# Kernel optimization log

Hardware: AMD Instinct MI355X
Metric: run time of the kernel (lower is better)

## Reference

```python
import jax, jax.numpy as jnp
import numpy as np
import math

B, L, D, H, DFF, NL = 32, 512, 768, 12, 3072, 2
E = D // H
VOCAB = 30522
TOPK = int(1 * math.log(L))   # factor=1 -> 6
MA = 25                        # series_decomp moving-average kernel (Autoformer default)
CMID = D // 2                  # 384 conv channels
PLEN = (L - 2) // 2            # 255 pooled length
LATENT, NCELLS = 32, 2034


def _ln(x, g, b, eps=1e-5):
    mu = x.mean(-1, keepdims=True)
    v = ((x - mu) ** 2).mean(-1, keepdims=True)
    return (x - mu) * jax.lax.rsqrt(v + eps) * g + b


def _decomp(x):
    # series_decomp: x - moving_avg(x, k=25) with replicate padding, via cumsum
    pad = (MA - 1) // 2
    xp = jnp.concatenate([jnp.repeat(x[:, :1], pad, 1), x, jnp.repeat(x[:, -1:], pad, 1)], 1)
    cs = jnp.cumsum(xp, axis=1)
    cs = jnp.concatenate([jnp.zeros_like(cs[:, :1]), cs], 1)
    mm = (cs[:, MA:] - cs[:, :-MA]) / MA  # [B,L,D]
    return x - mm


def _autocorr(q, k, v):
    # q,k,v: [B,L,H,E] -> FFT autocorrelation + top-k delay aggregation (inference path)
    qt = jnp.transpose(q, (0, 2, 3, 1))
    kt = jnp.transpose(k, (0, 2, 3, 1))
    vt = jnp.transpose(v, (0, 2, 3, 1))  # [B,H,E,L]
    corr = jnp.fft.irfft(jnp.fft.rfft(qt, axis=-1) * jnp.conj(jnp.fft.rfft(kt, axis=-1)), n=L, axis=-1)
    mean_value = corr.mean(axis=(1, 2))                      # [B,L]
    weights, delay = jax.lax.top_k(mean_value, TOPK)         # [B,K]
    w = jax.nn.softmax(weights, axis=-1)                     # [B,K]
    tv = jnp.concatenate([vt, vt], -1)                       # [B,H,E,2L]
    idx = jnp.arange(L)[None, None, :] + delay[:, :, None]   # [B,K,L]
    pat = jnp.take_along_axis(tv[:, None], idx[:, :, None, None, :], axis=-1)  # [B,K,H,E,L]
    V = jnp.einsum('bkhel,bk->bhel', pat, w)
    return jnp.transpose(V, (0, 3, 1, 2))                    # [B,L,H,E]


def _forward(input_ids, word_emb, pos_emb, tok_emb, emb_ln_g, emb_ln_b,
             Wq, bq, Wk, bk, Wv, bv, Wo, bo, Wc1, bc1, Wc2, bc2,
             norm_g, norm_b, conv_w, conv_b, bn_g, bn_b, bn_m, bn_v,
             lin1_w, lin1_b, ln2_g, ln2_b, lin2_w, lin2_b):
    # BertEmbeddings (token_type all zeros)
    x = word_emb[input_ids] + pos_emb[None, :L] + tok_emb[0][None, None]
    x = _ln(x, emb_ln_g, emb_ln_b, 1e-12)
    # Autoformer encoder layers
    for l in range(NL):
        q = (x @ Wq[l].T + bq[l]).reshape(B, L, H, E)
        k = (x @ Wk[l].T + bk[l]).reshape(B, L, H, E)
        v = (x @ Wv[l].T + bv[l]).reshape(B, L, H, E)
        a = _autocorr(q, k, v).reshape(B, L, D) @ Wo[l].T + bo[l]
        x = _decomp(x + a)
        y = jax.nn.gelu(x @ Wc1[l].T + bc1[l], approximate=False) @ Wc2[l].T + bc2[l]
        x = _decomp(x + y)
    # my_Layernorm
    x_hat = _ln(x, norm_g, norm_b)
    att_out = x_hat - x_hat.mean(axis=1, keepdims=True)      # [B,L,D]
    # Prediction head
    z = jnp.transpose(att_out, (0, 2, 1))                    # [B,D,L]
    c = jax.lax.conv_general_dilated(z, conv_w, (1,), 'VALID',
                                     dimension_numbers=('NCH', 'OIH', 'NCH')) + conv_b[None, :, None]
    c = (c - bn_m[None, :, None]) * jax.lax.rsqrt(bn_v + 1e-5)[None, :, None] * bn_g[None, :, None] + bn_b[None, :, None]
    c = jax.nn.elu(c)                                        # [B,384,510]
    p = c.reshape(B, CMID, PLEN, 2).max(-1)                  # maxpool k=2
    f = p.reshape(B, CMID * PLEN)
    h = jax.nn.elu(_ln(f @ lin1_w.T + lin1_b, ln2_g, ln2_b))
    return jax.nn.sigmoid(h @ lin2_w.T + lin2_b)             # [B,2034]


def setup_inputs() -> dict:
    key = jax.random.key(0)
    ks = iter(jax.random.split(key, 64))
    n = lambda *s: 0.02 * jax.random.normal(next(ks), s, dtype=jnp.float32)
    return dict(
        input_ids=jax.random.randint(next(ks), (B, L), 0, VOCAB),
        word_emb=n(VOCAB, D), pos_emb=n(L, D), tok_emb=n(2, D),
        emb_ln_g=jnp.ones((D,), jnp.float32), emb_ln_b=jnp.zeros((D,), jnp.float32),
        Wq=n(NL, D, D), bq=n(NL, D), Wk=n(NL, D, D), bk=n(NL, D),
        Wv=n(NL, D, D), bv=n(NL, D), Wo=n(NL, D, D), bo=n(NL, D),
        Wc1=n(NL, DFF, D), bc1=n(NL, DFF), Wc2=n(NL, D, DFF), bc2=n(NL, D),
        norm_g=jnp.ones((D,), jnp.float32), norm_b=jnp.zeros((D,), jnp.float32),
        conv_w=n(CMID, D, 3), conv_b=n(CMID),
        bn_g=jnp.ones((CMID,), jnp.float32), bn_b=jnp.zeros((CMID,), jnp.float32),
        bn_m=n(CMID), bn_v=jax.random.uniform(next(ks), (CMID,), jnp.float32) + 0.5,
        lin1_w=n(LATENT, CMID * PLEN), lin1_b=n(LATENT),
        ln2_g=jnp.ones((LATENT,), jnp.float32), ln2_b=jnp.zeros((LATENT,), jnp.float32),
        lin2_w=n(NCELLS, LATENT), lin2_b=n(NCELLS),
    )


def reference(input_ids, word_emb, pos_emb, tok_emb, emb_ln_g, emb_ln_b,
              Wq, bq, Wk, bk, Wv, bv, Wo, bo, Wc1, bc1, Wc2, bc2,
              norm_g, norm_b, conv_w, conv_b, bn_g, bn_b, bn_m, bn_v,
              lin1_w, lin1_b, ln2_g, ln2_b, lin2_w, lin2_b):
    return _forward(input_ids, word_emb, pos_emb, tok_emb, emb_ln_g, emb_ln_b,
                    Wq, bq, Wk, bk, Wv, bv, Wo, bo, Wc1, bc1, Wc2, bc2,
                    norm_g, norm_b, conv_w, conv_b, bn_g, bn_b, bn_m, bn_v,
                    lin1_w, lin1_b, ln2_g, ln2_b, lin2_w, lin2_b)
```

## Files before the change

kernel.cpp:

```cpp
#include <hip/hip_runtime.h>
#include <hip/hip_bf16.h>

#define B_ 32
#define L_ 512
#define D_ 768
#define DFF_ 3072
#define NL_ 2
#define TOPK_ 6
#define CMID_ 384
#define CLEN_ 510
#define PLEN_ 255
#define LATENT_ 32
#define NCELLS_ 2034
#define NROWS_ (B_*L_)
#define ND_ ((size_t)B_*L_*D_)

typedef unsigned short ushort_t;
typedef __attribute__((ext_vector_type(8))) short short8;
typedef __attribute__((ext_vector_type(4))) float f32x4;

typedef const __attribute__((address_space(1))) unsigned int* gp1;
typedef __attribute__((address_space(3))) unsigned int* lp3;

static __device__ __forceinline__ void gload16(const ushort_t* g, ushort_t* l) {
  __builtin_amdgcn_global_load_lds((gp1)g, (lp3)l, 16, 0, 0);
}

static __device__ __forceinline__ float geluf(float x) {
  return 0.5f * x * (1.f + erff(x * 0.70710678118654752440f));
}
static __device__ __forceinline__ float eluf(float x) {
  return x > 0.f ? x : expm1f(x);
}
static __device__ __forceinline__ ushort_t bf16rn(float f) {
  unsigned u = __builtin_bit_cast(unsigned, f);
  u = u + 0x7FFFu + ((u >> 16) & 1u);
  return (ushort_t)(u >> 16);
}
static __device__ __forceinline__ float bf16tof(ushort_t s) {
  unsigned u = ((unsigned)s) << 16;
  return __builtin_bit_cast(float, u);
}
static __device__ __forceinline__ f32x4 mfma16(short8 a, short8 b, f32x4 c) {
  return __builtin_amdgcn_mfma_f32_16x16x32_bf16(a, b, c, 0, 0, 0);
}

__global__ void wsplit(const float* __restrict__ w, ushort_t* __restrict__ hi,
                       ushort_t* __restrict__ lo, size_t n) {
  size_t stride = (size_t)gridDim.x * blockDim.x;
  for (size_t i = (size_t)blockIdx.x * blockDim.x + threadIdx.x; i < n; i += stride) {
    float v = w[i];
    ushort_t h = bf16rn(v);
    hi[i] = h;
    if (lo) lo[i] = bf16rn(v - bf16tof(h));
  }
}

__global__ __launch_bounds__(256) void tsplit(const float* __restrict__ in, ushort_t* __restrict__ hiT,
                                              ushort_t* __restrict__ loT) {
  __shared__ float tile[32][33];
  size_t off = (size_t)blockIdx.z * D_ * D_;
  int bx = blockIdx.x * 32, by = blockIdx.y * 32;
  int tx = threadIdx.x & 31, ty = threadIdx.x >> 5;
#pragma unroll
  for (int i = 0; i < 32; i += 8)
    tile[ty + i][tx] = in[off + (size_t)(by + ty + i) * D_ + bx + tx];
  __syncthreads();
#pragma unroll
  for (int i = 0; i < 32; i += 8) {
    float v = tile[tx][ty + i];
    ushort_t h = bf16rn(v);
    size_t o = off + (size_t)(bx + ty + i) * D_ + by + tx;
    hiT[o] = h;
    loT[o] = bf16rn(v - bf16tof(h));
  }
}

__global__ void bvo_k(const float* __restrict__ wo, const float* __restrict__ bv,
                      const float* __restrict__ bo, float* __restrict__ bvo) {
  int gid = blockIdx.x * 256 + threadIdx.x;
  if (gid >= NL_ * D_) return;
  int l = gid / D_, a = gid % D_;
  const float* w = wo + (size_t)l * D_ * D_ + (size_t)a * D_;
  const float* b = bv + l * D_;
  float s = bo[gid];
  for (int j = 0; j < D_; j++) s = fmaf(w[j], b[j], s);
  bvo[gid] = s;
}

__global__ void conv_w_repack(const float* __restrict__ w, ushort_t* __restrict__ wt) {
  int gid = blockIdx.x * blockDim.x + threadIdx.x;
  if (gid >= CMID_ * 3 * D_) return;
  int o = gid / (3 * D_);
  int k = gid % (3 * D_);
  int j = k / D_, i = k % D_;
  wt[gid] = bf16rn(w[((size_t)o * D_ + i) * 3 + j]);
}

__global__ __launch_bounds__(256) void embed_ln(const int* __restrict__ ids, const float* __restrict__ we,
                                                const float* __restrict__ pe, const float* __restrict__ te,
                                                const float* __restrict__ g, const float* __restrict__ bta,
                                                ushort_t* __restrict__ xh, ushort_t* __restrict__ xl) {
  int row = blockIdx.x;
  int tid = threadIdx.x;
  int t = row & (L_ - 1);
  int id = ids[row];
  float v[3];
#pragma unroll
  for (int dd = 0; dd < 3; dd++) {
    int c = tid + dd * 256;
    v[dd] = we[(size_t)id * D_ + c] + pe[(size_t)t * D_ + c] + te[c];
  }
  float s = v[0] + v[1] + v[2];
  float sq = v[0]*v[0] + v[1]*v[1] + v[2]*v[2];
  __shared__ float rs[256], rq[256];
  rs[tid] = s; rq[tid] = sq;
  __syncthreads();
  for (int st = 128; st > 0; st >>= 1) {
    if (tid < st) { rs[tid] += rs[tid + st]; rq[tid] += rq[tid + st]; }
    __syncthreads();
  }
  __shared__ float smu, ssc;
  if (tid == 0) {
    float mu = rs[0] * (1.f / D_);
    float var = fmaxf(rq[0] * (1.f / D_) - mu * mu, 0.f);
    smu = mu; ssc = rsqrtf(var + 1e-12f);
  }
  __syncthreads();
  float mu = smu, sc = ssc;
#pragma unroll
  for (int dd = 0; dd < 3; dd++) {
    int c = tid + dd * 256;
    size_t o = (size_t)row * D_ + c;
    float ov = (v[dd] - mu) * sc * g[c] + bta[c];
    ushort_t h = bf16rn(ov);
    xh[o] = h;
    xl[o] = bf16rn(ov - bf16tof(h));
  }
}

__global__ __launch_bounds__(256) void ln_pl(const ushort_t* __restrict__ xh, const ushort_t* __restrict__ xl,
                                             float* __restrict__ out,
                                             const float* __restrict__ g, const float* __restrict__ bta,
                                             float eps) {
  int row = blockIdx.x;
  int tid = threadIdx.x;
  size_t base = (size_t)row * D_;
  float v[3];
#pragma unroll
  for (int dd = 0; dd < 3; dd++) {
    size_t o = base + tid + dd * 256;
    v[dd] = bf16tof(xh[o]) + bf16tof(xl[o]);
  }
  float s = v[0] + v[1] + v[2];
  float sq = v[0]*v[0] + v[1]*v[1] + v[2]*v[2];
  __shared__ float rs[256], rq[256];
  rs[tid] = s; rq[tid] = sq;
  __syncthreads();
  for (int st = 128; st > 0; st >>= 1) {
    if (tid < st) { rs[tid] += rs[tid + st]; rq[tid] += rq[tid + st]; }
    __syncthreads();
  }
  __shared__ float smu, ssc;
  if (tid == 0) {
    float mu = rs[0] * (1.f / D_);
    float var = fmaxf(rq[0] * (1.f / D_) - mu * mu, 0.f);
    smu = mu; ssc = rsqrtf(var + eps);
  }
  __syncthreads();
  float mu = smu, sc = ssc;
  float* o = out + base;
#pragma unroll
  for (int dd = 0; dd < 3; dd++) {
    int c = tid + dd * 256;
    o[c] = (v[dd] - mu) * sc * g[c] + bta[c];
  }
}

template<int ACT, int EPI>
__global__ __launch_bounds__(512, 1) void gemm8p(
    const ushort_t* __restrict__ A, const ushort_t* __restrict__ W,
    const float* __restrict__ bias,
    const ushort_t* __restrict__ ResH, const ushort_t* __restrict__ ResL,
    void* __restrict__ C0, int O, int K, int lda, int nbx, int nby) {
  __shared__ __align__(16) ushort_t Asm[2][16384];
  __shared__ __align__(16) ushort_t Bsm[2][16384];

  int nwg = gridDim.x;
  int wg = blockIdx.x;
  {
    int qq = nwg >> 3, rr = nwg & 7;
    int xcd = wg & 7, idx = wg >> 3;
    wg = (xcd < rr ? xcd * (qq + 1) : rr * (qq + 1) + (xcd - rr) * qq) + idx;
  }
  int gsz = nbx * 8;
  int grp = wg / gsz;
  int ing = wg - grp * gsz;
  int by0 = grp * 8;
  int gmx = min(8, nby - by0);
  int by = by0 + (ing % gmx);
  int bx = ing / gmx;

  int m0 = by * 256, o0 = bx * 256;
  int tid = threadIdx.x;
  int wave = tid >> 6, lane = tid & 63;
  int wm = wave >> 2, wn = wave & 3;
  int lcol = lane & 15, lk = lane >> 4;
  int swzl = (lcol & 3) ^ ((lcol >> 2) & 3);
  int sloA = ((lk ^ swzl) << 3);
  int srcsw = (((tid & 3) ^ ((tid >> 2) & 3) ^ ((tid >> 4) & 3)) << 3);
  int nt = K >> 6;
  int niter = nt >> 1;

  f32x4 acc[8][4] = {};

  auto STAGE = [&](int T, int mat, int kh) {
    if (T >= nt) return;
    ushort_t* lb = (mat == 0 ? &Asm[T & 1][kh * 8192 + (wave << 9)]
                             : &Bsm[T & 1][kh * 8192 + (wave << 9)]);
    const ushort_t* gb = (mat == 0 ? A : W);
    int ld = (mat == 0 ? lda : K);
    int br = (mat == 0 ? m0 : o0) + (tid >> 2);
    int cc = T * 64 + kh * 32 + srcsw;
    gload16(gb + (size_t)br * ld + cc, lb);
    gload16(gb + (size_t)(br + 128) * ld + cc, lb + 4096);
  };

#define PHASE_(bufi, mh, kh, sT, sM, sK)                                         \
  {                                                                              \
    short8 af[4], bfr[4];                                                        \
    _Pragma("unroll")                                                            \
    for (int fi = 0; fi < 4; fi++)                                               \
      af[fi] = *(const short8*)&Asm[bufi][(kh) * 8192 +                          \
               (wm * 128 + (mh) * 64 + fi * 16 + lcol) * 32 + sloA];             \
    _Pragma("unroll")                                                            \
    for (int fj = 0; fj < 4; fj++)                                               \
      bfr[fj] = *(const short8*)&Bsm[bufi][(kh) * 8192 +                         \
               (wn * 64 + fj * 16 + lcol) * 32 + sloA];                          \
    STAGE(sT, sM, sK);                                                           \
    __builtin_amdgcn_s_barrier();                                                \
    asm volatile("s_waitcnt lgkmcnt(0)" ::: "memory");                           \
    __builtin_amdgcn_sched_barrier(0);                                           \
    __builtin_amdgcn_s_setprio(1);                                               \
    _Pragma("unroll")                                                            \
    for (int fi = 0; fi < 4; fi++)                                               \
      _Pragma("unroll")                                                          \
      for (int fj = 0; fj < 4; fj++)                                             \
        acc[(mh) * 4 + fi][fj] = mfma16(af[fi], bfr[fj], acc[(mh) * 4 + fi][fj]);\
    __builtin_amdgcn_s_setprio(0);                                               \
    __builtin_amdgcn_s_barrier();                                                \
  }

  STAGE(0, 0, 0); STAGE(0, 1, 0); STAGE(0, 0, 1); STAGE(0, 1, 1);
  STAGE(1, 0, 0); STAGE(1, 1, 0);

  for (int i = 0; i < niter; i++) {
    int E = 2 * i;
    asm volatile("s_waitcnt vmcnt(4)" ::: "memory");
    __builtin_amdgcn_s_barrier();
    PHASE_(0, 0, 0, E + 1, 0, 1);
    PHASE_(0, 1, 0, E + 1, 1, 1);
    PHASE_(0, 0, 1, E + 2, 0, 0);
    PHASE_(0, 1, 1, E + 2, 1, 0);
    if (i + 1 == niter) asm volatile("s_waitcnt vmcnt(0)" ::: "memory");
    else                asm volatile("s_waitcnt vmcnt(4)" ::: "memory");
    __builtin_amdgcn_s_barrier();
    PHASE_(1, 0, 0, E + 2, 0, 1);
    PHASE_(1, 1, 0, E + 2, 1, 1);
    PHASE_(1, 0, 1, E + 3, 0, 0);
    PHASE_(1, 1, 1, E + 3, 1, 0);
  }
#undef PHASE_

#pragma unroll
  for (int fi = 0; fi < 8; fi++) {
    int rowb = m0 + wm * 128 + fi * 16 + lk * 4;
#pragma unroll
    for (int fj = 0; fj < 4; fj++) {
      int col = o0 + wn * 64 + fj * 16 + lcol;
      float bv = bias ? bias[col] : 0.f;
#pragma unroll
      for (int r = 0; r < 4; r++) {
        float v = acc[fi][fj][r] + bv;
        if (ACT == 1) v = geluf(v);
        size_t off = (size_t)(rowb + r) * O + col;
        if (EPI == 0) {
          if (ResH) v += bf16tof(ResH[off]) + bf16tof(ResL[off]);
          ((float*)C0)[off] = v;
        }
        if (EPI == 1) ((ushort_t*)C0)[off] = bf16rn(v);
      }
    }
  }
}

template<int ACT, bool SPLIT, int EPI>
__global__ __launch_bounds__(256) void gemm_bf16(
    const ushort_t* __restrict__ Ah, const ushort_t* __restrict__ Al,
    const ushort_t* __restrict__ Wh, const ushort_t* __restrict__ Wl,
    const float* __restrict__ bias,
    const ushort_t* __restrict__ ResH, const ushort_t* __restrict__ ResL,
    void* __restrict__ C0, void* __restrict__ C1,
    const float* __restrict__ bn_m, const float* __restrict__ bn_v,
    const float* __restrict__ bn_g, const float* __restrict__ bn_b,
    int O, int K, int lda,
    long long sA, long long sW, long long sC,
    int nbx, int nby) {
  constexpr int NP = SPLIT ? 2 : 1;
  __shared__ __align__(16) ushort_t AsH[NP][128 * 64];
  __shared__ __align__(16) ushort_t WsH[NP][128 * 64];
  __shared__ float dsum[EPI == 3 ? 512 : 1];

  int nwg = gridDim.x;
  int wg = blockIdx.x;
  {
    int qq = nwg >> 3, rr = nwg & 7;
    int xcd = wg & 7, idx = wg >> 3;
    wg = (xcd < rr ? xcd * (qq + 1) : rr * (qq + 1) + (xcd - rr) * qq) + idx;
  }
  int per_b = nbx * nby;
  int bz = wg / per_b;
  int rem = wg - bz * per_b;
  int gsz = nbx * 8;
  int grp = rem / gsz;
  int ing = rem - grp * gsz;
  int by0 = grp * 8;
  int gmx = min(8, nby - by0);
  int by = by0 + (ing % gmx);
  int bx = ing / gmx;

  const ushort_t* Ahb = Ah + (size_t)bz * sA;
  const ushort_t* Alb = SPLIT ? (Al + (size_t)bz * sA) : nullptr;
  const ushort_t* Whb = Wh + (size_t)bz * sW;
  const ushort_t* Wlb = SPLIT ? (Wl + (size_t)bz * sW) : nullptr;

  int m0 = by * 128, o0 = bx * 128;
  int tid = threadIdx.x;
  int wave = tid >> 6, lane = tid & 63;
  int wm = (wave >> 1) * 64, wn = (wave & 1) * 64;
  int lcol = lane & 15, lk = lane >> 4;

  if (EPI == 3) {
    for (int s = tid; s < 512; s += 256) dsum[s] = 0.f;
  }

  f32x4 acc[4][4] = {};

  int r8 = lane >> 3;
  int kc = (((lane & 7) ^ r8) << 3);

  const ushort_t *gA[4], *gW[4], *gAl[4], *gWl[4];
#pragma unroll
  for (int i = 0; i < 4; i++) {
    int ch = wave * 4 + i;
    int row = ch * 8 + r8;
    size_t oa = (size_t)(m0 + row) * lda + kc;
    size_t ow = (size_t)(o0 + row) * K + kc;
    gA[i] = Ahb + oa; gW[i] = Whb + ow;
    if (SPLIT) { gAl[i] = Alb + oa; gWl[i] = Wlb + ow; }
  }

  for (int k0 = 0; k0 < K; k0 += 64) {
#pragma unroll
    for (int i = 0; i < 4; i++) {
      int ch = wave * 4 + i;
      gload16(gA[i], &AsH[0][ch * 512]); gA[i] += 64;
      gload16(gW[i], &WsH[0][ch * 512]); gW[i] += 64;
      if (SPLIT) {
        gload16(gAl[i], &AsH[1][ch * 512]); gAl[i] += 64;
        gload16(gWl[i], &WsH[1][ch * 512]); gWl[i] += 64;
      }
    }
    __syncthreads();
#pragma unroll
    for (int kk = 0; kk < 2; kk++) {
      int c = kk * 4 + lk;
      short8 ah[4], bh[4], al[4], bl[4];
#pragma unroll
      for (int i = 0; i < 4; i++) {
        int r = wm + i * 16 + lcol;
        int so = r * 64 + ((c ^ (r & 7)) << 3);
        ah[i] = *(const short8*)&AsH[0][so];
        if (SPLIT) al[i] = *(const short8*)&AsH[1][so];
      }
#pragma unroll
      for (int j = 0; j < 4; j++) {
        int r = wn + j * 16 + lcol;
        int so = r * 64 + ((c ^ (r & 7)) << 3);
        bh[j] = *(const short8*)&WsH[0][so];
        if (SPLIT) bl[j] = *(const short8*)&WsH[1][so];
      }
#pragma unroll
      for (int i = 0; i < 4; i++)
#pragma unroll
        for (int j = 0; j < 4; j++) {
          if (SPLIT) {
            acc[i][j] = mfma16(ah[i], bl[j], acc[i][j]);
            acc[i][j] = mfma16(al[i], bh[j], acc[i][j]);
          }
          acc[i][j] = mfma16(ah[i], bh[j], acc[i][j]);
        }
    }
    __syncthreads();
  }

  if (EPI == 3) {
    float pre[7][4] = {};
#pragma unroll
    for (int i = 0; i < 4; i++)
#pragma unroll
      for (int j = 0; j < 4; j++)
#pragma unroll
        for (int r = 0; r < 4; r++)
          pre[i - j + 3][r] += acc[i][j][r];
    int base = (m0 + wm + lk * 4) - (o0 + wn + lcol);
#pragma unroll
    for (int g = 0; g < 7; g++)
#pragma unroll
      for (int r = 0; r < 4; r++)
        atomicAdd(&dsum[(base + 16 * (g - 3) + r) & (L_ - 1)], pre[g][r]);
    __syncthreads();
    float* mvp = (float*)C0;
    int blk = by * nbx + bx;
    for (int s = tid; s < 512; s += 256)
      mvp[((size_t)bz * 16 + blk) * 512 + s] = dsum[s] * (1.f / D_);
  } else if (EPI == 4) {
#pragma unroll
    for (int j = 0; j < 4; j++) {
      int col = o0 + wn + j * 16 + lcol;
      float cbias = bias[col];
      float sc = rsqrtf(bn_v[col] + 1e-5f) * bn_g[col];
      float shf = bn_b[col] - bn_m[col] * sc;
#pragma unroll
      for (int i = 0; i < 4; i++) {
        int rowb = m0 + wm + i * 16 + lk * 4;
        int t = rowb & (L_ - 1);
        int b = rowb >> 9;
#pragma unroll
        for (int p = 0; p < 2; p++) {
          int tt = t + p * 2;
          if (tt >= CLEN_) continue;
          float v0 = eluf((acc[i][j][p * 2]     + cbias) * sc + shf);
          float v1 = eluf((acc[i][j][p * 2 + 1] + cbias) * sc + shf);
          ((float*)C0)[((size_t)b * CMID_ + col) * PLEN_ + (tt >> 1)] = fmaxf(v0, v1);
        }
      }
    }
  } else {
#pragma unroll
    for (int i = 0; i < 4; i++)
#pragma unroll
      for (int j = 0; j < 4; j++) {
        int col = o0 + wn + j * 16 + lcol;
        float bv = bias ? bias[col] : 0.f;
        int rowb = m0 + wm + i * 16 + lk * 4;
#pragma unroll
        for (int r = 0; r < 4; r++) {
          float v = acc[i][j][r] + bv;
          if (ACT == 1) v = geluf(v);
          size_t off = (size_t)bz * sC + (size_t)(rowb + r) * O + col;
          if (EPI == 0) {
            if (ResH) v += bf16tof(ResH[off]) + bf16tof(ResL[off]);
            ((float*)C0)[off] = v;
          }
          if (EPI == 1) ((ushort_t*)C0)[off] = bf16rn(v);
          if (EPI == 2) {
            ushort_t h = bf16rn(v);
            ((ushort_t*)C0)[off] = h;
            ((ushort_t*)C1)[off] = bf16rn(v - bf16tof(h));
          }
        }
      }
  }
}

__global__ __launch_bounds__(256) void topk_softmax(const float* __restrict__ mvp,
                                                    float* __restrict__ wout, int* __restrict__ dout) {
  int b = blockIdx.x, tid = threadIdx.x;
  __shared__ float vals[L_];
  __shared__ float rv[256];
  __shared__ int ri[256];
  __shared__ float wsel[TOPK_];
  __shared__ int dsel[TOPK_];
  float s0 = 0.f, s1 = 0.f;
  for (int p = 0; p < 16; p++) {
    const float* pp = mvp + ((size_t)b * 16 + p) * L_;
    s0 += pp[tid]; s1 += pp[tid + 256];
  }
  vals[tid] = s0; vals[tid + 256] = s1;
  for (int kk = 0; kk < TOPK_; kk++) {
    __syncthreads();
    float v0 = vals[tid], v1 = vals[tid + 256];
    float bvv = v0; int bi = tid;
    if (v1 > v0) { bvv = v1; bi = tid + 256; }
    rv[tid] = bvv; ri[tid] = bi;
    __syncthreads();
    for (int st = 128; st > 0; st >>= 1) {
      if (tid < st) {
        float ov = rv[tid + st]; int oi = ri[tid + st];
        if (ov > rv[tid] || (ov == rv[tid] && oi < ri[tid])) { rv[tid] = ov; ri[tid] = oi; }
      }
      __syncthreads();
    }
    if (tid == 0) { wsel[kk] = rv[0]; dsel[kk] = ri[0]; vals[ri[0]] = -INFINITY; }
  }
  __syncthreads();
  if (tid == 0) {
    float mx = wsel[0];
    for (int i = 1; i < TOPK_; i++) mx = fmaxf(mx, wsel[i]);
    float e[TOPK_]; float sum = 0.f;
    for (int i = 0; i < TOPK_; i++) { e[i] = expf(wsel[i] - mx); sum += e[i]; }
    for (int i = 0; i < TOPK_; i++) { wout[b * TOPK_ + i] = e[i] / sum; dout[b * TOPK_ + i] = dsel[i]; }
  }
}

__global__ __launch_bounds__(256) void agg_res(const ushort_t* __restrict__ P, const float* __restrict__ w,
                                               const int* __restrict__ dly,
                                               const ushort_t* __restrict__ xh, const ushort_t* __restrict__ xl,
                                               float* __restrict__ y) {
  int blr = blockIdx.x;
  int b = blr >> 9, t = blr & 511;
  int tid = threadIdx.x;
  __shared__ float ww[TOPK_];
  __shared__ int rr[TOPK_];
  if (tid < TOPK_) { ww[tid] = w[b * TOPK_ + tid]; rr[tid] = (t + dly[b * TOPK_ + tid]) & (L_ - 1); }
  __syncthreads();
  const ushort_t* pb = P + (size_t)b * L_ * D_;
#pragma unroll
  for (int dd = 0; dd < 3; dd++) {
    int d = tid + dd * 256;
    size_t o = (size_t)blr * D_ + d;
    float s = bf16tof(xh[o]) + bf16tof(xl[o]);
#pragma unroll
    for (int kk = 0; kk < TOPK_; kk++)
      s = fmaf(ww[kk], bf16tof(pb[(size_t)rr[kk] * D_ + d]), s);
    y[o] = s;
  }
}

__global__ void decomp_pl(const float* __restrict__ s,
                          ushort_t* __restrict__ xh, ushort_t* __restrict__ xl) {
  int gid = blockIdx.x * blockDim.x + threadIdx.x;
  if (gid >= B_ * 8 * D_) return;
  int d = gid % D_;
  int chunk = (gid / D_) & 7;
  int b = gid / (D_ * 8);
  size_t base = (size_t)b * L_ * D_ + d;
  int t0 = chunk * 64;
  float wsum = 0.f;
  for (int u = t0 - 12; u <= t0 + 12; u++) {
    int uc = u < 0 ? 0 : (u > L_ - 1 ? L_ - 1 : u);
    wsum += s[base + (size_t)uc * D_];
  }
  for (int t = t0; t < t0 + 64; t++) {
    size_t o = base + (size_t)t * D_;
    float v = s[o] - wsum * (1.f / 25.f);
    ushort_t h = bf16rn(v);
    xh[o] = h;
    xl[o] = bf16rn(v - bf16tof(h));
    int ua = t + 13 > L_ - 1 ? L_ - 1 : t + 13;
    int ur = t - 12 < 0 ? 0 : t - 12;
    wsum += s[base + (size_t)ua * D_] - s[base + (size_t)ur * D_];
  }
}

__global__ void colmean_bf16(const float* __restrict__ x, ushort_t* __restrict__ sh) {
  int gid = blockIdx.x * blockDim.x + threadIdx.x;
  if (gid >= B_ * D_) return;
  int d = gid % D_, b = gid / D_;
  const float* col = x + (size_t)b * L_ * D_ + d;
  ushort_t* oc = sh + (size_t)b * L_ * D_ + d;
  float s = 0.f;
  for (int t = 0; t < L_; t++) s += col[(size_t)t * D_];
  float mu = s * (1.f / L_);
  for (int t = 0; t < L_; t++) oc[(size_t)t * D_] = bf16rn(col[(size_t)t * D_] - mu);
}

__global__ __launch_bounds__(256) void lin1_k(const float* __restrict__ f, const float* __restrict__ w,
                                              const float* __restrict__ bias, float* __restrict__ out) {
  int o = blockIdx.x, b = blockIdx.y;
  int tid = threadIdx.x;
  const float4* fr = (const float4*)(f + (size_t)b * (CMID_ * PLEN_));
  const float4* wr = (const float4*)(w + (size_t)o * (CMID_ * PLEN_));
  const int n4 = CMID_ * PLEN_ / 4;
  float s = 0.f;
  for (int i = tid; i < n4; i += 256) {
    float4 a = fr[i], ww = wr[i];
    s += a.x * ww.x + a.y * ww.y + a.z * ww.z + a.w * ww.w;
  }
  __shared__ float red[256];
  red[tid] = s;
  __syncthreads();
  for (int st = 128; st > 0; st >>= 1) {
    if (tid < st) red[tid] += red[tid + st];
    __syncthreads();
  }
  if (tid == 0) out[b * LATENT_ + o] = red[0] + bias[o];
}

__global__ void ln_elu(const float* __restrict__ hp, const float* __restrict__ g,
                       const float* __restrict__ bb, float* __restrict__ h) {
  int b = blockIdx.x;
  int tid = threadIdx.x;
  __shared__ float v[LATENT_];
  __shared__ float mu_s, sc_s;
  if (tid < LATENT_) v[tid] = hp[b * LATENT_ + tid];
  __syncthreads();
  if (tid == 0) {
    float s = 0.f, sq = 0.f;
    for (int i = 0; i < LATENT_; i++) { s += v[i]; sq += v[i] * v[i]; }
    float mu = s * (1.f / LATENT_);
    float var = fmaxf(sq * (1.f / LATENT_) - mu * mu, 0.f);
    mu_s = mu; sc_s = rsqrtf(var + 1e-5f);
  }
  __syncthreads();
  if (tid < LATENT_) h[b * LATENT_ + tid] = eluf((v[tid] - mu_s) * sc_s * g[tid] + bb[tid]);
}

__global__ void lin2_sig(const float* __restrict__ h, const float* __restrict__ w,
                         const float* __restrict__ bias, float* __restrict__ out) {
  int gid = blockIdx.x * blockDim.x + threadIdx.x;
  if (gid >= B_ * NCELLS_) return;
  int b = gid / NCELLS_, c = gid % NCELLS_;
  const float* hr = h + b * LATENT_;
  const float* wr = w + (size_t)c * LATENT_;
  float s = bias[c];
  for (int j = 0; j < LATENT_; j++) s = fmaf(hr[j], wr[j], s);
  out[gid] = 1.f / (1.f + expf(-s));
}

extern "C" void kernel_launch(void* const* d_in, const int* in_sizes, int n_in,
                              void* d_out, int out_size, void* d_ws, size_t ws_size,
                              hipStream_t stream) {
  const int*   ids  = (const int*)  d_in[0];
  const float* we   = (const float*)d_in[1];
  const float* pe   = (const float*)d_in[2];
  const float* te   = (const float*)d_in[3];
  const float* elng = (const float*)d_in[4];
  const float* elnb = (const float*)d_in[5];
  const float* Wq   = (const float*)d_in[6];
  const float* bq   = (const float*)d_in[7];   (void)bq;
  const float* Wk   = (const float*)d_in[8];
  const float* bk   = (const float*)d_in[9];   (void)bk;
  const float* Wv   = (const float*)d_in[10];
  const float* bv   = (const float*)d_in[11];
  const float* Wo   = (const float*)d_in[12];
  const float* bo   = (const float*)d_in[13];
  const float* Wc1  = (const float*)d_in[14];
  const float* bc1  = (const float*)d_in[15];
  const float* Wc2  = (const float*)d_in[16];
  const float* bc2  = (const float*)d_in[17];
  const float* ng   = (const float*)d_in[18];
  const float* nb   = (const float*)d_in[19];
  const float* cw   = (const float*)d_in[20];
  const float* cb   = (const float*)d_in[21];
  const float* bng  = (const float*)d_in[22];
  const float* bnb  = (const float*)d_in[23];
  const float* bnm  = (const float*)d_in[24];
  const float* bnv  = (const float*)d_in[25];
  const float* l1w  = (const float*)d_in[26];
  const float* l1b  = (const float*)d_in[27];
  const float* l2g  = (const float*)d_in[28];
  const float* l2b  = (const float*)d_in[29];
  const float* l2w  = (const float*)d_in[30];
  const float* l2bi = (const float*)d_in[31];
  float* out = (float*)d_out;

  char* wp = (char*)d_ws;
  auto alloc = [&](size_t bytes) { char* p = wp; wp += (bytes + 255) & ~(size_t)255; return p; };
  ushort_t* Xh  = (ushort_t*)alloc(ND_ * 2);
  ushort_t* Xl  = (ushort_t*)alloc(ND_ * 2);
  ushort_t* R1  = (ushort_t*)alloc(ND_ * 2 * 4);
  char*     PvB = (char*)    alloc(ND_ * 4);
  float*    Y   = (float*)   alloc(ND_ * 4);
  float*    MVP = (float*)   alloc((size_t)B_ * 16 * L_ * 4);
  float*    WT  = (float*)   alloc(B_ * TOPK_ * 4);
  int*      DT  = (int*)     alloc(B_ * TOPK_ * 4);
  float*    HP  = (float*)   alloc(B_ * LATENT_ * 4);
  float*    HH  = (float*)   alloc(B_ * LATENT_ * 4);
  const size_t DD = (size_t)D_ * D_, DF = (size_t)DFF_ * D_;
  ushort_t* MTh  = (ushort_t*)alloc(NL_ * DD * 2);
  ushort_t* MTl  = (ushort_t*)alloc(NL_ * DD * 2);
  ushort_t* WvoH = (ushort_t*)alloc(NL_ * DD * 2);
  float*    BVO  = (float*)   alloc(NL_ * D_ * 4);
  ushort_t* W1H  = (ushort_t*)alloc(NL_ * DF * 2);
  ushort_t* W2H  = (ushort_t*)alloc(NL_ * DF * 2);
  ushort_t* WTC  = (ushort_t*)alloc((size_t)CMID_ * 3 * D_ * 2);

  ushort_t* XMh = R1;
  ushort_t* XMl = R1 + ND_;
  ushort_t* Gh  = R1;
  float*    F   = (float*)R1;
  ushort_t* Pb  = (ushort_t*)PvB;
  float*    LNo = (float*)PvB;
  ushort_t* Sh  = Xh;

  ushort_t* SC = R1;
  ushort_t* WqTh = SC;                ushort_t* WqTl = SC + 1 * NL_ * DD;
  ushort_t* WkTh = SC + 2 * NL_ * DD; ushort_t* WkTl = SC + 3 * NL_ * DD;
  ushort_t* WvTh = SC + 4 * NL_ * DD; ushort_t* WvTl = SC + 5 * NL_ * DD;
  ushort_t* WoH  = SC + 6 * NL_ * DD; ushort_t* WoL  = SC + 7 * NL_ * DD;

  tsplit<<<dim3(24, 24, NL_), 256, 0, stream>>>(Wq, WqTh, WqTl);
  tsplit<<<dim3(24, 24, NL_), 256, 0, stream>>>(Wk, WkTh, WkTl);
  tsplit<<<dim3(24, 24, NL_), 256, 0, stream>>>(Wv, WvTh, WvTl);
  wsplit<<<512, 256, 0, stream>>>(Wo, WoH, WoL, NL_ * DD);
  wsplit<<<1024, 256, 0, stream>>>(Wc1, W1H, nullptr, NL_ * DF);
  wsplit<<<1024, 256, 0, stream>>>(Wc2, W2H, nullptr, NL_ * DF);
  conv_w_repack<<<(CMID_ * 3 * D_ + 255) / 256, 256, 0, stream>>>(cw, WTC);

  gemm_bf16<0, true, 2><<<72, 256, 0, stream>>>(WkTh, WkTl, WqTh, WqTl, nullptr, nullptr, nullptr,
                                                MTh, MTl, nullptr, nullptr, nullptr, nullptr,
                                                D_, D_, D_, (long long)DD, (long long)DD, (long long)DD, 6, 6);
  gemm_bf16<0, true, 1><<<72, 256, 0, stream>>>(WoH, WoL, WvTh, WvTl, nullptr, nullptr, nullptr,
                                                WvoH, nullptr, nullptr, nullptr, nullptr, nullptr,
                                                D_, D_, D_, (long long)DD, (long long)DD, (long long)DD, 6, 6);
  bvo_k<<<(NL_ * D_ + 255) / 256, 256, 0, stream>>>(Wo, bv, bo, BVO);

  embed_ln<<<NROWS_, 256, 0, stream>>>(ids, we, pe, te, elng, elnb, Xh, Xl);

  for (int l = 0; l < NL_; l++) {
    gemm_bf16<0, true, 2><<<768, 256, 0, stream>>>(Xh, Xl, MTh + l*DD, MTl + l*DD, nullptr, nullptr, nullptr,
                                                   XMh, XMl, nullptr, nullptr, nullptr, nullptr,
                                                   D_, D_, D_, 0, 0, 0, 6, 128);
    gemm8p<0, 1><<<192, 512, 0, stream>>>(Xh, WvoH + l*DD, BVO + l*D_, nullptr, nullptr,
                                          Pb, D_, D_, D_, 3, 64);
    gemm_bf16<0, true, 3><<<512, 256, 0, stream>>>(XMh, XMl, Xh, Xl, nullptr, nullptr, nullptr,
                                                   MVP, nullptr, nullptr, nullptr, nullptr, nullptr,
                                                   L_, D_, D_, (long long)L_ * D_, (long long)L_ * D_, 0, 4, 4);
    topk_softmax<<<B_, 256, 0, stream>>>(MVP, WT, DT);
    agg_res<<<NROWS_, 256, 0, stream>>>(Pb, WT, DT, Xh, Xl, Y);
    decomp_pl<<<(B_ * 8 * D_) / 256, 256, 0, stream>>>(Y, Xh, Xl);
    gemm8p<1, 1><<<768, 512, 0, stream>>>(Xh, W1H + l*DF, bc1 + l*DFF_, nullptr, nullptr,
                                          Gh, DFF_, D_, D_, 12, 64);
    gemm8p<0, 0><<<192, 512, 0, stream>>>(Gh, W2H + l*DF, bc2 + l*D_, Xh, Xl,
                                          Y, D_, DFF_, DFF_, 3, 64);
    decomp_pl<<<(B_ * 8 * D_) / 256, 256, 0, stream>>>(Y, Xh, Xl);
  }

  ln_pl<<<NROWS_, 256, 0, stream>>>(Xh, Xl, LNo, ng, nb, 1e-5f);
  colmean_bf16<<<(B_ * D_ + 255) / 256, 256, 0, stream>>>(LNo, Sh);

  gemm_bf16<0, false, 4><<<384, 256, 0, stream>>>(Sh, nullptr, WTC, nullptr, cb, nullptr, nullptr,
                                                  F, nullptr, bnm, bnv, bng, bnb,
                                                  CMID_, 3 * D_, D_, 0, 0, 0, 3, 128);
  lin1_k<<<dim3(LATENT_, B_), 256, 0, stream>>>(F, l1w, l1b, HP);
  ln_elu<<<B_, 64, 0, stream>>>(HP, l2g, l2b, HH);
  lin2_sig<<<(B_ * NCELLS_ + 255) / 256, 256, 0, stream>>>(HH, l2w, l2bi, out);
}
```

Baseline: 1.371 ms.

## Store full 64-wide K rows in LDS with XOR swizzle and single-tile pipeline

The bf16 GEMM previously held each 64-wide K tile in shared memory as two separate 32-column halves. It now keeps 256x64 rows contiguous with an 8-chunk XOR swizzle, so each global load fetches 128 contiguous bytes per row. The main loop is restructured to process one K tile per iteration, issuing the four staging units for the next tile across the four compute phases with adjusted vmcnt waits. The aim is better global-load coalescing and conflict-free LDS fragment reads. The risk is that the new prefetch schedule exposes more load latency than the previous two-tile unrolled pipeline.

```diff
diff --git a/kernel.cpp b/kernel.cpp
--- a/kernel.cpp
+++ b/kernel.cpp
@@ -183,8 +183,8 @@
     const float* __restrict__ bias,
     const ushort_t* __restrict__ ResH, const ushort_t* __restrict__ ResL,
     void* __restrict__ C0, int O, int K, int lda, int nbx, int nby) {
-  __shared__ __align__(16) ushort_t Asm[2][16384];
-  __shared__ __align__(16) ushort_t Bsm[2][16384];
+  __shared__ __align__(16) ushort_t Asm[2][256 * 64];
+  __shared__ __align__(16) ushort_t Bsm[2][256 * 64];
 
   int nwg = gridDim.x;
   int wg = blockIdx.x;
@@ -206,38 +206,40 @@
   int wave = tid >> 6, lane = tid & 63;
   int wm = wave >> 2, wn = wave & 3;
   int lcol = lane & 15, lk = lane >> 4;
-  int swzl = (lcol & 3) ^ ((lcol >> 2) & 3);
-  int sloA = ((lk ^ swzl) << 3);
-  int srcsw = (((tid & 3) ^ ((tid >> 2) & 3) ^ ((tid >> 4) & 3)) << 3);
+  int r8l = lane >> 3;
+  int kc = (((lane & 7) ^ r8l) << 3);
   int nt = K >> 6;
-  int niter = nt >> 1;
 
   f32x4 acc[8][4] = {};
 
-  auto STAGE = [&](int T, int mat, int kh) {
+  auto STAGE = [&](int T, int u) {
     if (T >= nt) return;
-    ushort_t* lb = (mat == 0 ? &Asm[T & 1][kh * 8192 + (wave << 9)]
-                             : &Bsm[T & 1][kh * 8192 + (wave << 9)]);
+    int mat = u >> 1, uh = u & 1;
+    ushort_t* lb = (mat == 0 ? Asm[T & 1] : Bsm[T & 1]) + uh * 8192 + wave * 512;
     const ushort_t* gb = (mat == 0 ? A : W);
     int ld = (mat == 0 ? lda : K);
-    int br = (mat == 0 ? m0 : o0) + (tid >> 2);
-    int cc = T * 64 + kh * 32 + srcsw;
+    int br = (mat == 0 ? m0 : o0) + uh * 128 + wave * 8 + r8l;
+    int cc = T * 64 + kc;
     gload16(gb + (size_t)br * ld + cc, lb);
-    gload16(gb + (size_t)(br + 128) * ld + cc, lb + 4096);
+    gload16(gb + (size_t)(br + 64) * ld + cc, lb + 4096);
   };
 
-#define PHASE_(bufi, mh, kh, sT, sM, sK)                                         \
+#define PHASE_(bufi, mh, kh, sT, sU)                                             \
   {                                                                              \
     short8 af[4], bfr[4];                                                        \
     _Pragma("unroll")                                                            \
-    for (int fi = 0; fi < 4; fi++)                                               \
-      af[fi] = *(const short8*)&Asm[bufi][(kh) * 8192 +                          \
-               (wm * 128 + (mh) * 64 + fi * 16 + lcol) * 32 + sloA];             \
+    for (int fi = 0; fi < 4; fi++) {                                             \
+      int ra = wm * 128 + (mh) * 64 + fi * 16 + lcol;                            \
+      af[fi] = *(const short8*)&Asm[bufi][ra * 64 +                              \
+               ((((kh) * 4 + lk) ^ (lcol & 7)) << 3)];                           \
+    }                                                                            \
     _Pragma("unroll")                                                            \
-    for (int fj = 0; fj < 4; fj++)                                               \
-      bfr[fj] = *(const short8*)&Bsm[bufi][(kh) * 8192 +                         \
-               (wn * 64 + fj * 16 + lcol) * 32 + sloA];                          \
-    STAGE(sT, sM, sK);                                                           \
+    for (int fj = 0; fj < 4; fj++) {                                             \
+      int rb = wn * 64 + fj * 16 + lcol;                                         \
+      bfr[fj] = *(const short8*)&Bsm[bufi][rb * 64 +                             \
+               ((((kh) * 4 + lk) ^ (lcol & 7)) << 3)];                           \
+    }                                                                            \
+    if ((sU) >= 0) STAGE(sT, sU);                                                \
     __builtin_amdgcn_s_barrier();                                                \
     asm volatile("s_waitcnt lgkmcnt(0)" ::: "memory");                           \
     __builtin_amdgcn_sched_barrier(0);                                           \
@@ -251,24 +253,18 @@
     __builtin_amdgcn_s_barrier();                                                \
   }
 
-  STAGE(0, 0, 0); STAGE(0, 1, 0); STAGE(0, 0, 1); STAGE(0, 1, 1);
-  STAGE(1, 0, 0); STAGE(1, 1, 0);
-
-  for (int i = 0; i < niter; i++) {
-    int E = 2 * i;
-    asm volatile("s_waitcnt vmcnt(4)" ::: "memory");
+  STAGE(0, 0); STAGE(0, 1); STAGE(0, 2); STAGE(0, 3);
+
+  for (int T = 0; T < nt; T++) {
+    int buf = T & 1;
+    STAGE(T + 1, 0);
+    if (T + 1 < nt) asm volatile("s_waitcnt vmcnt(2)" ::: "memory");
+    else            asm volatile("s_waitcnt vmcnt(0)" ::: "memory");
     __builtin_amdgcn_s_barrier();
-    PHASE_(0, 0, 0, E + 1, 0, 1);
-    PHASE_(0, 1, 0, E + 1, 1, 1);
-    PHASE_(0, 0, 1, E + 2, 0, 0);
-    PHASE_(0, 1, 1, E + 2, 1, 0);
-    if (i + 1 == niter) asm volatile("s_waitcnt vmcnt(0)" ::: "memory");
-    else                asm volatile("s_waitcnt vmcnt(4)" ::: "memory");
-    __builtin_amdgcn_s_barrier();
-    PHASE_(1, 0, 0, E + 2, 0, 1);
-    PHASE_(1, 1, 0, E + 2, 1, 1);
-    PHASE_(1, 0, 1, E + 3, 0, 0);
-    PHASE_(1, 1, 1, E + 3, 1, 0);
+    PHASE_(buf, 0, 0, T + 1, 1);
+    PHASE_(buf, 0, 1, T + 1, 2);
+    PHASE_(buf, 1, 0, T + 1, 3);
+    PHASE_(buf, 1, 1, -1, -1);
   }
 #undef PHASE_
 
```

Result: no change. 1.376 ms (+0.4%).
